# Kernel tuning notes

Hardware: AMD Instinct MI355X
Metric: run time of the kernel (lower is better)

Reference implementation:

```python
import jax, jax.numpy as jnp
import numpy as np


def _to_patch_vectors(x, batch_size, patch_size, img_size):
    # x: (B, 1, H, W) -> (N, s*s) with N = B*(H/s)^2, row-major patch order
    # (outer loop over patch rows m, inner loop over patch cols n), scaled by 1/100
    s = patch_size
    g = img_size // s
    x = x.reshape(batch_size, g, s, g, s)          # (B, gm, s, gn, s)
    x = x.transpose(0, 1, 3, 2, 4)                 # (B, gm, gn, s, s)
    return x.reshape(batch_size * g * g, s * s) / 100.0


def _le_loss2(pred_vec, maps_vec, n_neighbors):
    # Exact kNN on maps_vec (Euclidean), equivalent to sklearn ball_tree exact search.
    N = maps_vec.shape[0]
    sq = jnp.sum(maps_vec * maps_vec, axis=-1)                     # (N,)
    D = sq[:, None] + sq[None, :] - 2.0 * (maps_vec @ maps_vec.T)  # (N, N) squared dists
    _, idx = jax.lax.top_k(-D, n_neighbors)                        # (N, k) nearest (incl. self)

    nbr = maps_vec[idx]                                            # (N, k, d)
    diff = maps_vec[:, None, :] - nbr
    d_l2 = jnp.sqrt(jnp.sum(diff * diff, axis=-1))                 # (N, k)
    d_l1 = jnp.sum(jnp.abs(diff), axis=-1) + 1e-8                  # (N, k)
    w = jnp.exp(-d_l2 / d_l1)                                      # sparse W entries, N*k nonzeros

    # W has exactly these N*k nonzeros (top_k indices are unique per row),
    # so sum_{i,j} ||pred_i - pred_j|| * W[i,j] reduces to the neighbor pairs only.
    pdiff = pred_vec[:, None, :] - pred_vec[idx]                   # (N, k, d)
    pd = jnp.sqrt(jnp.maximum(jnp.sum(pdiff * pdiff, axis=-1), 0.0))
    return jnp.sum(pd * w) / (N * N)


def setup_inputs() -> dict:
    key = jax.random.key(0)
    k1, k2, k3 = jax.random.split(key, 3)
    B, H = 32, 256
    return {
        "pred": jax.random.normal(k1, (B, 1, H, H), dtype=jnp.float32),
        "maps": jax.random.normal(k2, (B, 1, H, H), dtype=jnp.float32),
        "img": jax.random.normal(k3, (B, 1, H, H), dtype=jnp.float32),
        "lamda": jnp.ones((), dtype=jnp.float32),
        "batch_size": B,
        "patch_size": 16,
        "img_size": H,
        "n_neighbors": 10,
    }


def reference(pred, maps, img, lamda, batch_size, patch_size, img_size, n_neighbors):
    pred_vec = _to_patch_vectors(pred, batch_size, patch_size, img_size)
    maps_vec = _to_patch_vectors(maps, batch_size, patch_size, img_size)
    loss2 = _le_loss2(pred_vec, maps_vec, n_neighbors)
    mse = jnp.mean((maps - pred) ** 2)
    return jnp.sum(mse + loss2 * lamda)
```

## Files before the change

### kernel.cpp

```cpp
#include <hip/hip_runtime.h>
#include <math.h>

#define N_ROWS 8192
#define DIM    256
#define KNN    10

typedef __attribute__((ext_vector_type(8))) short bf16x8;
typedef __attribute__((ext_vector_type(4))) float f32x4;

__device__ __forceinline__ unsigned short f2bf(float f) {
    unsigned u = __float_as_uint(f);
    return (unsigned short)((u + 0x7fff + ((u >> 16) & 1)) >> 16);
}
__device__ __forceinline__ float bf2f(unsigned short b) {
    return __uint_as_float(((unsigned)b) << 16);
}

__device__ __forceinline__ void gl16(const unsigned short* gp, unsigned short* lp) {
    __builtin_amdgcn_global_load_lds(
        (const __attribute__((address_space(1))) unsigned int*)gp,
        (__attribute__((address_space(3))) unsigned int*)lp,
        16, 0, 0);
}

__device__ __forceinline__ void ins10(unsigned (&t)[KNN], unsigned v) {
#pragma unroll
    for (int q = 0; q < KNN; ++q) {
        unsigned lo = min(t[q], v);
        v = max(t[q], v);
        t[q] = lo;
    }
}

__device__ __forceinline__ void merge10(unsigned (&a)[KNN], const unsigned (&b)[KNN]) {
    unsigned o[KNN];
#pragma unroll
    for (int i = 0; i < KNN; ++i) {
        unsigned best = min(a[i], b[i]);
#pragma unroll
        for (int j = 0; j < i; ++j)
            best = min(best, max(a[j], b[i - 1 - j]));
        o[i] = best;
    }
#pragma unroll
    for (int i = 0; i < KNN; ++i) a[i] = o[i];
}

__global__ __launch_bounds__(256) void k_extract(const float* __restrict__ pred,
                                                 const float* __restrict__ maps,
                                                 unsigned short* __restrict__ mapsB,
                                                 unsigned short* __restrict__ predB,
                                                 float* __restrict__ sqn,
                                                 float* __restrict__ msePart) {
    const int row = blockIdx.x * 4 + (threadIdx.x >> 6);
    const int l   = threadIdx.x & 63;
    const int b = row >> 8, m = (row >> 4) & 15, n = row & 15;
    const int r = l >> 2, cb = (l & 3) * 4;
    const int src = (b << 16) + ((m * 16 + r) << 8) + (n * 16 + cb);

    const float4 p4 = *reinterpret_cast<const float4*>(&pred[src]);
    const float4 q4 = *reinterpret_cast<const float4*>(&maps[src]);

    ushort4 mv4, pv4;
    mv4.x = f2bf(q4.x * 0.01f); mv4.y = f2bf(q4.y * 0.01f);
    mv4.z = f2bf(q4.z * 0.01f); mv4.w = f2bf(q4.w * 0.01f);
    pv4.x = f2bf(p4.x * 0.01f); pv4.y = f2bf(p4.y * 0.01f);
    pv4.z = f2bf(p4.z * 0.01f); pv4.w = f2bf(p4.w * 0.01f);
    *reinterpret_cast<ushort4*>(&mapsB[row * DIM + l * 4]) = mv4;
    *reinterpret_cast<ushort4*>(&predB[row * DIM + l * 4]) = pv4;

    float m0 = bf2f(mv4.x), m1 = bf2f(mv4.y), m2 = bf2f(mv4.z), m3 = bf2f(mv4.w);
    float sq = m0 * m0 + m1 * m1 + m2 * m2 + m3 * m3;
    float d0 = q4.x - p4.x, d1 = q4.y - p4.y, d2 = q4.z - p4.z, d3 = q4.w - p4.w;
    float ms = d0 * d0 + d1 * d1 + d2 * d2 + d3 * d3;

    for (int off = 32; off; off >>= 1) {
        sq += __shfl_down(sq, off);
        ms += __shfl_down(ms, off);
    }
    if (l == 0) {
        sqn[row] = sq;
        msePart[row] = ms;
    }
}

__global__ __launch_bounds__(512, 4) void k_knn(const unsigned short* __restrict__ mapsB,
                                                const float* __restrict__ sqn,
                                                unsigned int* __restrict__ part) {
    __shared__ unsigned short Bs[128 * 64];
    __shared__ float SJQf[1024];

    const int tid = threadIdx.x;
    const int l   = tid & 63;
    const int w   = tid >> 6;
    const int i0  = blockIdx.x * 128;
    const int js0 = blockIdx.y * 1024;
    const int l15 = l & 15;
    const int l4  = l >> 4;
    const int c7  = l15 & 7;
    int bBase[8];
#pragma unroll
    for (int nn = 0; nn < 8; ++nn) bBase[nn] = (nn * 16 + l15) * 64;

    bf16x8 af[8];
    {
        const unsigned short* arow = &mapsB[(i0 + w * 16 + l15) * DIM + l4 * 8];
#pragma unroll
        for (int i = 0; i < 8; ++i)
            af[i] = *reinterpret_cast<const bf16x8*>(&arow[i * 32]);
    }

    const unsigned short *bSrc0, *bSrc1;
    {
        int c, r, c8;
        c = w * 128 + l;        r = c >> 3; c8 = c & 7;
        bSrc0 = mapsB + (js0 + r) * DIM + ((c8 ^ (r & 7)) << 3);
        c = w * 128 + 64 + l;   r = c >> 3; c8 = c & 7;
        bSrc1 = mapsB + (js0 + r) * DIM + ((c8 ^ (r & 7)) << 3);
    }
    unsigned short* bDst0 = &Bs[(w * 128) * 8];
    unsigned short* bDst1 = &Bs[(w * 128 + 64) * 8];

    for (int e = tid; e < 1024; e += 512)
        SJQf[e] = fmaf(sqn[js0 + e], 131072.f, 32768.f);

    unsigned tops[4][KNN];
#pragma unroll
    for (int q = 0; q < 4; ++q)
#pragma unroll
        for (int ss = 0; ss < KNN; ++ss) tops[q][ss] = 0xFFFFFFFFu;

#pragma unroll 1
    for (int tt = 0; tt < 8; ++tt) {
        const int jg0  = js0 + tt * 128;
        const int jOff = tt * 128 * DIM;

        f32x4 acc[8];
#pragma unroll
        for (int nn = 0; nn < 8; ++nn)
#pragma unroll
            for (int q = 0; q < 4; ++q) acc[nn][q] = 0.f;

#pragma unroll
        for (int kt = 0; kt < 4; ++kt) {
            const int k0 = kt * 64;
            __syncthreads();
            gl16(bSrc0 + jOff + k0, bDst0);
            gl16(bSrc1 + jOff + k0, bDst1);
            __syncthreads();

#pragma unroll
            for (int g = 0; g < 2; ++g) {
                const int kb = g * 4 + l4;
                const int swz = (kb ^ c7) << 3;
                const bf16x8 a = af[kt * 2 + g];
#pragma unroll
                for (int h = 0; h < 2; ++h) {
                    bf16x8 b0 = *reinterpret_cast<const bf16x8*>(&Bs[bBase[h * 4 + 0] + swz]);
                    bf16x8 b1 = *reinterpret_cast<const bf16x8*>(&Bs[bBase[h * 4 + 1] + swz]);
                    bf16x8 b2 = *reinterpret_cast<const bf16x8*>(&Bs[bBase[h * 4 + 2] + swz]);
                    bf16x8 b3 = *reinterpret_cast<const bf16x8*>(&Bs[bBase[h * 4 + 3] + swz]);
                    acc[h * 4 + 0] = __builtin_amdgcn_mfma_f32_16x16x32_bf16(a, b0, acc[h * 4 + 0], 0, 0, 0);
                    acc[h * 4 + 1] = __builtin_amdgcn_mfma_f32_16x16x32_bf16(a, b1, acc[h * 4 + 1], 0, 0, 0);
                    acc[h * 4 + 2] = __builtin_amdgcn_mfma_f32_16x16x32_bf16(a, b2, acc[h * 4 + 2], 0, 0, 0);
                    acc[h * 4 + 3] = __builtin_amdgcn_mfma_f32_16x16x32_bf16(a, b3, acc[h * 4 + 3], 0, 0, 0);
                }
            }
        }

        float sj[8]; unsigned jc[8];
#pragma unroll
        for (int nn = 0; nn < 8; ++nn) {
            sj[nn] = SJQf[tt * 128 + nn * 16 + l15];
            jc[nn] = (unsigned)(jg0 + nn * 16 + l15);
        }
#pragma unroll
        for (int q = 0; q < 4; ++q) {
            unsigned c[8];
#pragma unroll
            for (int nn = 0; nn < 8; ++nn) {
                unsigned u = __float2uint_rn(fmaf(acc[nn][q], -262144.f, sj[nn]));
                c[nn] = (u << 16) | jc[nn];
            }
            unsigned win = min(min(min(c[0], c[1]), min(c[2], c[3])),
                               min(min(c[4], c[5]), min(c[6], c[7])));
            ins10(tops[q], win);
        }
    }

#pragma unroll
    for (int q = 0; q < 4; ++q) {
#pragma unroll
        for (int off = 1; off <= 8; off <<= 1) {
            unsigned ob[KNN];
#pragma unroll
            for (int ss = 0; ss < KNN; ++ss)
                ob[ss] = (unsigned)__shfl_xor((int)tops[q][ss], off);
            merge10(tops[q], ob);
        }
    }
    if (l15 == 0) {
        const int rbase = i0 + w * 16 + l4 * 4;
#pragma unroll
        for (int q = 0; q < 4; ++q)
#pragma unroll
            for (int ss = 0; ss < KNN; ++ss)
                part[(rbase + q) * (8 * KNN) + blockIdx.y * KNN + ss] = tops[q][ss];
    }
}

__global__ __launch_bounds__(256) void k_mp(const unsigned short* __restrict__ mapsB,
                                            const unsigned short* __restrict__ predB,
                                            const unsigned int* __restrict__ part,
                                            float* __restrict__ pairPart) {
    const int row = blockIdx.x * 4 + (threadIdx.x >> 6);
    const int l   = threadIdx.x & 63;

    unsigned t[KNN];
    {
        unsigned e0 = part[row * (8 * KNN) + l];
        unsigned e1 = (l < 16) ? part[row * (8 * KNN) + 64 + l] : 0xFFFFFFFFu;
        t[0] = min(e0, e1);
        t[1] = max(e0, e1);
#pragma unroll
        for (int ss = 2; ss < KNN; ++ss) t[ss] = 0xFFFFFFFFu;
    }
#pragma unroll
    for (int off = 1; off <= 32; off <<= 1) {
        unsigned ob[KNN];
#pragma unroll
        for (int ss = 0; ss < KNN; ++ss)
            ob[ss] = (unsigned)__shfl_xor((int)t[ss], off);
        merge10(t, ob);
    }

    const ushort4 m4 = *reinterpret_cast<const ushort4*>(&mapsB[row * DIM + l * 4]);
    const ushort4 p4 = *reinterpret_cast<const ushort4*>(&predB[row * DIM + l * 4]);
    float mi[4] = { bf2f(m4.x), bf2f(m4.y), bf2f(m4.z), bf2f(m4.w) };
    float pi[4] = { bf2f(p4.x), bf2f(p4.y), bf2f(p4.z), bf2f(p4.w) };

    float wsum = 0.f;
#pragma unroll 2
    for (int nb = 0; nb < KNN; ++nb) {
        const int jj = (int)(t[nb] & 0xFFFFu);
        const ushort4 mj4 = *reinterpret_cast<const ushort4*>(&mapsB[jj * DIM + l * 4]);
        const ushort4 pj4 = *reinterpret_cast<const ushort4*>(&predB[jj * DIM + l * 4]);
        float s2m = 0.f, s1m = 0.f, s2p = 0.f;
        float mj[4] = { bf2f(mj4.x), bf2f(mj4.y), bf2f(mj4.z), bf2f(mj4.w) };
        float pj[4] = { bf2f(pj4.x), bf2f(pj4.y), bf2f(pj4.z), bf2f(pj4.w) };
#pragma unroll
        for (int e = 0; e < 4; ++e) {
            float dm = mi[e] - mj[e];
            float dp = pi[e] - pj[e];
            s2m = fmaf(dm, dm, s2m);
            s1m += fabsf(dm);
            s2p = fmaf(dp, dp, s2p);
        }
        for (int off = 32; off; off >>= 1) {
            s2m += __shfl_down(s2m, off);
            s1m += __shfl_down(s1m, off);
            s2p += __shfl_down(s2p, off);
        }
        if (l == 0) {
            float d2  = sqrtf(s2m);
            float d1  = s1m + 1e-8f;
            float wgt = expf(-d2 / d1);
            float pd  = sqrtf(fmaxf(s2p, 0.f));
            wsum += pd * wgt;
        }
    }
    if (l == 0) pairPart[row] = wsum;
}

__global__ __launch_bounds__(256) void k_final(const float* __restrict__ msePart,
                                               const float* __restrict__ pairPart,
                                               const float* __restrict__ lamda,
                                               float* __restrict__ out) {
    const int tid = threadIdx.x;
    float sm = 0.f, sp = 0.f;
    for (int i = tid; i < N_ROWS; i += 256) { sm += msePart[i]; sp += pairPart[i]; }
    for (int off = 32; off; off >>= 1) {
        sm += __shfl_down(sm, off);
        sp += __shfl_down(sp, off);
    }
    __shared__ float s_m[4], s_p[4];
    int wave = tid >> 6;
    if ((tid & 63) == 0) { s_m[wave] = sm; s_p[wave] = sp; }
    __syncthreads();
    if (tid == 0) {
        float mse   = (s_m[0] + s_m[1] + s_m[2] + s_m[3]) / 2097152.0f;
        float loss2 = (s_p[0] + s_p[1] + s_p[2] + s_p[3]) / (8192.0f * 8192.0f);
        out[0] = mse + loss2 * lamda[0];
    }
}

extern "C" void kernel_launch(void* const* d_in, const int* in_sizes, int n_in,
                              void* d_out, int out_size, void* d_ws, size_t ws_size,
                              hipStream_t stream) {
    const float* pred  = (const float*)d_in[0];
    const float* maps  = (const float*)d_in[1];
    const float* lamda = (const float*)d_in[3];
    float* out = (float*)d_out;

    char* W = (char*)d_ws;
    unsigned short* mapsB = (unsigned short*)W;
    unsigned short* predB = (unsigned short*)(W + 4194304);
    float* sqn       = (float*)(W + 8388608);
    float* msePart   = (float*)(W + 8388608 + 32768);
    float* pairPart  = (float*)(W + 8388608 + 65536);
    unsigned int* part = (unsigned int*)(W + 8388608 + 98304);

    k_extract<<<dim3(N_ROWS / 4), dim3(256), 0, stream>>>(pred, maps, mapsB, predB, sqn, msePart);
    k_knn<<<dim3(N_ROWS / 128, 8), dim3(512), 0, stream>>>(mapsB, sqn, part);
    k_mp<<<dim3(N_ROWS / 4), dim3(256), 0, stream>>>(mapsB, predB, part, pairPart);
    k_final<<<dim3(1), dim3(256), 0, stream>>>(msePart, pairPart, lamda, out);
}
```

Baseline: 102.0 us.

## Widen kNN K-tile to 128 and split neighbor gather across two waves

The kNN GEMM now stages 128-wide K slices of B in LDS instead of 64, which halves the number of barrier pairs per j-tile and changes the XOR swizzle to 16 chunks. The per-row neighbor kernel now gives each row two waves, each handling five of the ten neighbors, and combines their partial sums through shared memory. The first change doubles LDS per block, which may reduce occupancy. The second doubles the grid to expose more parallelism for the latency-bound gathers, at the cost of redundant top-k merging in both waves.

```diff
diff --git a/kernel.cpp b/kernel.cpp
--- a/kernel.cpp
+++ b/kernel.cpp
@@ -87,7 +87,7 @@
 __global__ __launch_bounds__(512, 4) void k_knn(const unsigned short* __restrict__ mapsB,
                                                 const float* __restrict__ sqn,
                                                 unsigned int* __restrict__ part) {
-    __shared__ unsigned short Bs[128 * 64];
+    __shared__ unsigned short Bs[128 * 128];
     __shared__ float SJQf[1024];
 
     const int tid = threadIdx.x;
@@ -97,10 +97,9 @@
     const int js0 = blockIdx.y * 1024;
     const int l15 = l & 15;
     const int l4  = l >> 4;
-    const int c7  = l15 & 7;
     int bBase[8];
 #pragma unroll
-    for (int nn = 0; nn < 8; ++nn) bBase[nn] = (nn * 16 + l15) * 64;
+    for (int nn = 0; nn < 8; ++nn) bBase[nn] = (nn * 16 + l15) * 128;
 
     bf16x8 af[8];
     {
@@ -110,16 +109,22 @@
             af[i] = *reinterpret_cast<const bf16x8*>(&arow[i * 32]);
     }
 
-    const unsigned short *bSrc0, *bSrc1;
+    const unsigned short *bSrc0, *bSrc1, *bSrc2, *bSrc3;
     {
-        int c, r, c8;
-        c = w * 128 + l;        r = c >> 3; c8 = c & 7;
-        bSrc0 = mapsB + (js0 + r) * DIM + ((c8 ^ (r & 7)) << 3);
-        c = w * 128 + 64 + l;   r = c >> 3; c8 = c & 7;
-        bSrc1 = mapsB + (js0 + r) * DIM + ((c8 ^ (r & 7)) << 3);
-    }
-    unsigned short* bDst0 = &Bs[(w * 128) * 8];
-    unsigned short* bDst1 = &Bs[(w * 128 + 64) * 8];
+        int c, r, c16;
+        c = w * 256 + l;        r = c >> 4; c16 = c & 15;
+        bSrc0 = mapsB + (js0 + r) * DIM + ((c16 ^ (r & 15)) << 3);
+        c = w * 256 + 64 + l;   r = c >> 4; c16 = c & 15;
+        bSrc1 = mapsB + (js0 + r) * DIM + ((c16 ^ (r & 15)) << 3);
+        c = w * 256 + 128 + l;  r = c >> 4; c16 = c & 15;
+        bSrc2 = mapsB + (js0 + r) * DIM + ((c16 ^ (r & 15)) << 3);
+        c = w * 256 + 192 + l;  r = c >> 4; c16 = c & 15;
+        bSrc3 = mapsB + (js0 + r) * DIM + ((c16 ^ (r & 15)) << 3);
+    }
+    unsigned short* bDst0 = &Bs[(w * 256) * 8];
+    unsigned short* bDst1 = &Bs[(w * 256 + 64) * 8];
+    unsigned short* bDst2 = &Bs[(w * 256 + 128) * 8];
+    unsigned short* bDst3 = &Bs[(w * 256 + 192) * 8];
 
     for (int e = tid; e < 1024; e += 512)
         SJQf[e] = fmaf(sqn[js0 + e], 131072.f, 32768.f);
@@ -142,18 +147,20 @@
             for (int q = 0; q < 4; ++q) acc[nn][q] = 0.f;
 
 #pragma unroll
-        for (int kt = 0; kt < 4; ++kt) {
-            const int k0 = kt * 64;
+        for (int kh = 0; kh < 2; ++kh) {
+            const int k0 = kh * 128;
             __syncthreads();
             gl16(bSrc0 + jOff + k0, bDst0);
             gl16(bSrc1 + jOff + k0, bDst1);
+            gl16(bSrc2 + jOff + k0, bDst2);
+            gl16(bSrc3 + jOff + k0, bDst3);
             __syncthreads();
 
 #pragma unroll
-            for (int g = 0; g < 2; ++g) {
-                const int kb = g * 4 + l4;
-                const int swz = (kb ^ c7) << 3;
-                const bf16x8 a = af[kt * 2 + g];
+            for (int kk = 0; kk < 4; ++kk) {
+                const int kb = kk * 4 + l4;
+                const int swz = (kb ^ l15) << 3;
+                const bf16x8 a = af[kh * 4 + kk];
 #pragma unroll
                 for (int h = 0; h < 2; ++h) {
                     bf16x8 b0 = *reinterpret_cast<const bf16x8*>(&Bs[bBase[h * 4 + 0] + swz]);
@@ -213,8 +220,10 @@
                                             const unsigned short* __restrict__ predB,
                                             const unsigned int* __restrict__ part,
                                             float* __restrict__ pairPart) {
-    const int row = blockIdx.x * 4 + (threadIdx.x >> 6);
-    const int l   = threadIdx.x & 63;
+    const int w    = threadIdx.x >> 6;
+    const int row  = blockIdx.x * 2 + (w >> 1);
+    const int half = w & 1;
+    const int l    = threadIdx.x & 63;
 
     unsigned t[KNN];
     {
@@ -240,9 +249,10 @@
     float pi[4] = { bf2f(p4.x), bf2f(p4.y), bf2f(p4.z), bf2f(p4.w) };
 
     float wsum = 0.f;
-#pragma unroll 2
-    for (int nb = 0; nb < KNN; ++nb) {
-        const int jj = (int)(t[nb] & 0xFFFFu);
+#pragma unroll
+    for (int k = 0; k < 5; ++k) {
+        const unsigned tn = half ? t[k + 5] : t[k];
+        const int jj = (int)(tn & 0xFFFFu);
         const ushort4 mj4 = *reinterpret_cast<const ushort4*>(&mapsB[jj * DIM + l * 4]);
         const ushort4 pj4 = *reinterpret_cast<const ushort4*>(&predB[jj * DIM + l * 4]);
         float s2m = 0.f, s1m = 0.f, s2p = 0.f;
@@ -269,7 +279,10 @@
             wsum += pd * wgt;
         }
     }
-    if (l == 0) pairPart[row] = wsum;
+    __shared__ float wsums[4];
+    if (l == 0) wsums[w] = wsum;
+    __syncthreads();
+    if (l == 0 && half == 0) pairPart[row] = wsums[w] + wsums[w + 1];
 }
 
 __global__ __launch_bounds__(256) void k_final(const float* __restrict__ msePart,
@@ -312,6 +325,6 @@
 
     k_extract<<<dim3(N_ROWS / 4), dim3(256), 0, stream>>>(pred, maps, mapsB, predB, sqn, msePart);
     k_knn<<<dim3(N_ROWS / 128, 8), dim3(512), 0, stream>>>(mapsB, sqn, part);
-    k_mp<<<dim3(N_ROWS / 4), dim3(256), 0, stream>>>(mapsB, predB, part, pairPart);
+    k_mp<<<dim3(N_ROWS / 2), dim3(256), 0, stream>>>(mapsB, predB, part, pairPart);
     k_final<<<dim3(1), dim3(256), 0, stream>>>(msePart, pairPart, lamda, out);
 }
```

After: 109.6 us. 1.07x slower.
